# Kernel tuning notes

Hardware: AMD Instinct MI355X
Metric: run time of the kernel (lower is better)

## Reference

```python
import jax, jax.numpy as jnp
import numpy as np

N, IN, M = 8192, 512, 512


def setup_inputs() -> dict:
    key = jax.random.key(0)
    ks = jax.random.split(key, 16)
    sI = 1.0 / np.sqrt(IN)
    sM = 1.0 / np.sqrt(M)
    def p(k, shape, scale):
        return jax.random.uniform(k, shape, jnp.float32, -scale, scale)
    # topologically sorted tree: parent[i] < i for i>0; root (i=0) points to sentinel N
    rng = np.random.default_rng(0)
    parent = (rng.random(N) * np.arange(N)).astype(np.int64)
    parent[0] = N
    return {
        "inputs": jax.random.normal(ks[0], (N, IN), jnp.float32),
        "parent": jnp.asarray(parent),
        # FPChildSumTreeLSTM params (bottom-up)
        "cs_Wx": p(ks[1], (5 * M, IN), sI), "cs_bx": p(ks[2], (5 * M,), sI),
        "cs_Wio": p(ks[3], (2 * M, M), sM), "cs_bio": p(ks[4], (2 * M,), sM),
        "cs_Wfz": p(ks[5], (2 * M, M), sM), "cs_bfz": p(ks[6], (2 * M,), sM),
        "cs_Wum": p(ks[7], (M, M), sM), "cs_bum": p(ks[8], (M,), sM),
        # FPChainTreeLSTM params (top-down)
        "ch_Wx": p(ks[9], (5 * M, IN), sI), "ch_bx": p(ks[10], (5 * M,), sI),
        "ch_Wh": p(ks[11], (4 * M, M), sM), "ch_bh": p(ks[12], (4 * M,), sM),
        "ch_Wum": p(ks[13], (M, M), sM), "ch_bum": p(ks[14], (M,), sM),
    }


def _childsum(inputs, parent, Wx, bx, Wio, bio, Wfz, bfz, Wum, bum):
    # Precompute input projections for all nodes at once; row N is a zero sentinel.
    px = inputs @ Wx.T + bx                                  # (N, 5M)
    px = jnp.concatenate([px, jnp.zeros((1, 5 * M), px.dtype)], axis=0)
    ix, fx, ox, zx, ux = (px[:, j * M:(j + 1) * M] for j in range(5))
    # Process nodes leaves->root (reverse topo order). Each finished node j
    # scatters its parent-dependent contributions into accumulators at parent[j]:
    #   acc_h  += h_j
    #   acc_fc += sigmoid(fx_parent + U_f h_j + b_f) * c_j
    #   acc_zc += sigmoid(zx_parent + U_z h_j + b_z) * tanh(c_j)
    # Leaves see zero accumulators, which exactly matches the torch zero phantom child.
    zero = jnp.zeros((N + 1, M), inputs.dtype)

    def step(carry, i):
        acc_h, acc_fc, acc_zc = carry
        io = acc_h[i] @ Wio.T + bio                          # (2M,)
        i_g = jax.nn.sigmoid(ix[i] + io[:M])
        o_g = jax.nn.sigmoid(ox[i] + io[M:])
        u = jnp.tanh(ux[i] + acc_zc[i] @ Wum.T + bum)
        c = i_g * u + acc_fc[i]
        h = o_g * jnp.tanh(c)
        p = parent[i]                                        # root -> sentinel N
        fz = h @ Wfz.T + bfz
        f = jax.nn.sigmoid(fx[p] + fz[:M])
        z = jax.nn.sigmoid(zx[p] + fz[M:])
        acc_h = acc_h.at[p].add(h)
        acc_fc = acc_fc.at[p].add(f * c)
        acc_zc = acc_zc.at[p].add(z * jnp.tanh(c))
        return (acc_h, acc_fc, acc_zc), h

    _, hs = jax.lax.scan(step, (zero, zero, zero), jnp.arange(N - 1, -1, -1))
    return hs[-1]                                            # root hidden, (M,)


def _chain(inputs, parent, Wx, bx, Wh, bh, Wum, bum):
    qx = inputs @ Wx.T + bx                                  # (N, 5M), order i,o,f,z,u
    ix, ox, fx, zx, ux = (qx[:, j * M:(j + 1) * M] for j in range(5))
    zero = jnp.zeros((N + 1, M), inputs.dtype)               # slot N = root's zero parent

    def step(carry, i):
        c_all, h_all = carry
        p = parent[i]
        pc, ph = c_all[p], h_all[p]
        g = ph @ Wh.T + bh                                   # (4M,), order i,o,f,z
        i_g = jax.nn.sigmoid(ix[i] + g[:M])
        o_g = jax.nn.sigmoid(ox[i] + g[M:2 * M])
        f_g = jax.nn.sigmoid(fx[i] + g[2 * M:3 * M])
        z_g = jax.nn.sigmoid(zx[i] + g[3 * M:])
        u = jnp.tanh(ux[i] + (z_g * jnp.tanh(pc)) @ Wum.T + bum)
        c = i_g * u + f_g * pc
        h = o_g * jnp.tanh(c)
        return (c_all.at[i].set(c), h_all.at[i].set(h)), None

    (_, h_all), _ = jax.lax.scan(step, (zero, zero), jnp.arange(N))
    return jnp.max(h_all[:N], axis=0)                        # max over all node hiddens, (M,)


def reference(inputs, parent, cs_Wx, cs_bx, cs_Wio, cs_bio, cs_Wfz, cs_bfz,
              cs_Wum, cs_bum, ch_Wx, ch_bx, ch_Wh, ch_bh, ch_Wum, ch_bum):
    frep = _childsum(inputs, parent, cs_Wx, cs_bx, cs_Wio, cs_bio,
                     cs_Wfz, cs_bfz, cs_Wum, cs_bum)
    brep = _chain(inputs, parent, ch_Wx, ch_bx, ch_Wh, ch_bh, ch_Wum, ch_bum)
    return jnp.concatenate([frep, brep])[None, :]            # (1, 2M)
```

## Files before the change

kernel.cpp:

```cpp
#include <hip/hip_runtime.h>
#include <hip/hip_cooperative_groups.h>
#include <hip/hip_bf16.h>

typedef unsigned short u16;
typedef unsigned int u32;
typedef unsigned long long u64;

#define NN 8192
#define PXC 2560
#define MAXD 36
#define GY 64
#define GYM 32

typedef __attribute__((ext_vector_type(8))) short bf16x8;
typedef __attribute__((ext_vector_type(4))) float f32x4;

static constexpr size_t SZ_PX  = (size_t)(NN + 1) * PXC * 2;
static constexpr size_t SZ_ACC = (size_t)(NN + 1) * 512 * 4;
static constexpr size_t SZ_HB  = (size_t)(NN + 1) * 512 * 2;
static constexpr size_t SZ_G   = (size_t)(NN + 1) * 1536 * 4;
static constexpr size_t SZ_NW  = (size_t)5242880 * 2;

static constexpr size_t OFF_PX    = 0;
static constexpr size_t OFF_QX    = OFF_PX + SZ_PX;
static constexpr size_t OFF_ACCH  = OFF_QX + SZ_PX;
static constexpr size_t OFF_ACCF  = OFF_ACCH + SZ_ACC;
static constexpr size_t OFF_ACCZ  = OFF_ACCF + SZ_ACC;
static constexpr size_t OFF_C     = OFF_ACCZ + SZ_ACC;
static constexpr size_t OFF_HB    = OFF_C + SZ_ACC;
static constexpr size_t OFF_ZB    = OFF_HB + SZ_HB;
static constexpr size_t OFF_G     = OFF_ZB + SZ_HB;
static constexpr size_t OFF_NW    = OFF_G + SZ_G;
static constexpr size_t OFF_DEPTH = OFF_NW + SZ_NW;
static constexpr size_t OFF_ORDER = OFF_DEPTH + (size_t)NN * 4;
static constexpr size_t OFF_MISC  = OFF_ORDER + (size_t)NN * 4;
static constexpr size_t OFF_LVL   = OFF_MISC + 1024;
static constexpr size_t OFF_NB    = OFF_LVL + 512;
static constexpr size_t OFF_PN    = OFF_NB + 20480;
static constexpr size_t OFF_PMAX  = OFF_PN + (size_t)NN * 4;
static constexpr size_t OFF_BAR   = OFF_PMAX + (size_t)128 * 512 * 4;
static constexpr size_t WS_TOTAL  = OFF_BAR + 32768;

#define NW_CSWX  0
#define NW_CHWX  1310720
#define NW_CSWIO 2621440
#define NW_CSWFZ 3145728
#define NW_CSWUM 3670016
#define NW_CHWH  3932160
#define NW_CHWUM 4980736

#define NB_CSBX  0
#define NB_CSBIO 2560
#define NB_CSBFZ 3584
#define NB_CSBUM 4608
#define NB_CHBX  5120
#define NB_CHBH  7680
#define NB_CHBUM 9728

__device__ __forceinline__ float bfu(u16 u) { return __uint_as_float(((u32)u) << 16); }
__device__ __forceinline__ u16 f2bf(float f) {
    u32 u = __float_as_uint(f);
    u += 0x7fffu + ((u >> 16) & 1u);
    return (u16)(u >> 16);
}
__device__ __forceinline__ float sigf(float x) {
    x = fminf(fmaxf(x, -30.f), 30.f);
    return 1.f / (1.f + __expf(-x));
}
__device__ __forceinline__ float tanhq(float x) {
    x = fminf(fmaxf(x, -15.f), 15.f);
    return 1.f - 2.f / (__expf(2.f * x) + 1.f);
}
__device__ __forceinline__ bf16x8 cvt8(const float* p) {
    float4 a = *(const float4*)p;
    float4 b = *(const float4*)(p + 4);
    union { u32 u[4]; bf16x8 v; } r;
    r.u[0] = ((__float_as_uint(a.x) + 0x8000u) >> 16) | ((__float_as_uint(a.y) + 0x8000u) & 0xffff0000u);
    r.u[1] = ((__float_as_uint(a.z) + 0x8000u) >> 16) | ((__float_as_uint(a.w) + 0x8000u) & 0xffff0000u);
    r.u[2] = ((__float_as_uint(b.x) + 0x8000u) >> 16) | ((__float_as_uint(b.y) + 0x8000u) & 0xffff0000u);
    r.u[3] = ((__float_as_uint(b.z) + 0x8000u) >> 16) | ((__float_as_uint(b.w) + 0x8000u) & 0xffff0000u);
    return r.v;
}

__device__ __forceinline__ u64 cld64(const void* p) {
    return __hip_atomic_load((const u64*)p, __ATOMIC_RELAXED, __HIP_MEMORY_SCOPE_AGENT);
}
__device__ __forceinline__ float cldf(const float* p) {
    return __hip_atomic_load(p, __ATOMIC_RELAXED, __HIP_MEMORY_SCOPE_AGENT);
}
__device__ __forceinline__ void cstf(float* p, float v) {
    __hip_atomic_store(p, v, __ATOMIC_RELAXED, __HIP_MEMORY_SCOPE_AGENT);
}
__device__ __forceinline__ void cst16(u16* p, u16 v) {
    __hip_atomic_store(p, v, __ATOMIC_RELAXED, __HIP_MEMORY_SCOPE_AGENT);
}
__device__ __forceinline__ bf16x8 cldb16(const u16* p) {
    union { u64 u[2]; bf16x8 v; } r;
    r.u[0] = cld64(p); r.u[1] = cld64(p + 4);
    return r.v;
}
__device__ __forceinline__ bf16x8 cvt8a(const float* p) {
    union { u64 u; u32 w[2]; } a, b, c, d;
    a.u = cld64(p); b.u = cld64(p + 2); c.u = cld64(p + 4); d.u = cld64(p + 6);
    union { u32 u[4]; bf16x8 v; } r;
    r.u[0] = ((a.w[0] + 0x8000u) >> 16) | ((a.w[1] + 0x8000u) & 0xffff0000u);
    r.u[1] = ((b.w[0] + 0x8000u) >> 16) | ((b.w[1] + 0x8000u) & 0xffff0000u);
    r.u[2] = ((c.w[0] + 0x8000u) >> 16) | ((c.w[1] + 0x8000u) & 0xffff0000u);
    r.u[3] = ((d.w[0] + 0x8000u) >> 16) | ((d.w[1] + 0x8000u) & 0xffff0000u);
    return r.v;
}

__device__ __forceinline__ void grid_bar(u32* B, int bid, u32 tgt) {
    __syncthreads();
    if (threadIdx.x == 0) {
        u32* leaf = B + (bid & 7) * 16;
        u32* root = B + 128;
        u32* gen  = B + 144;
        bool rel = false;
        u32 lo = __hip_atomic_fetch_add(leaf, 1u, __ATOMIC_RELAXED, __HIP_MEMORY_SCOPE_AGENT);
        if (lo == 31u) {
            __hip_atomic_store(leaf, 0u, __ATOMIC_RELAXED, __HIP_MEMORY_SCOPE_AGENT);
            u32 ro = __hip_atomic_fetch_add(root, 1u, __ATOMIC_RELAXED, __HIP_MEMORY_SCOPE_AGENT);
            if (ro == 7u) {
                __hip_atomic_store(root, 0u, __ATOMIC_RELAXED, __HIP_MEMORY_SCOPE_AGENT);
                __hip_atomic_store(gen, tgt, __ATOMIC_RELAXED, __HIP_MEMORY_SCOPE_AGENT);
                rel = true;
            }
        }
        if (!rel) {
            while (__hip_atomic_load(gen, __ATOMIC_RELAXED, __HIP_MEMORY_SCOPE_AGENT) < tgt)
                __builtin_amdgcn_s_sleep(1);
        }
        asm volatile("" ::: "memory");
    }
    __syncthreads();
}

__device__ __forceinline__ void mini_bar(u32* C, u32 tgt) {
    __syncthreads();
    if (threadIdx.x == 0) {
        __hip_atomic_fetch_add(C, 1u, __ATOMIC_RELAXED, __HIP_MEMORY_SCOPE_AGENT);
        while (__hip_atomic_load(C, __ATOMIC_RELAXED, __HIP_MEMORY_SCOPE_AGENT) < tgt)
            __builtin_amdgcn_s_sleep(1);
        asm volatile("" ::: "memory");
    }
    __syncthreads();
}

__global__ void k_detect(const u32* __restrict__ fin, const u32* __restrict__ pin,
                         int* __restrict__ fcnt, int* __restrict__ pcnt,
                         u32* __restrict__ barz) {
    int i = blockIdx.x * 256 + threadIdx.x;
    if (i < 8192) barz[i] = 0u;
    if (i < 4096) {
        u32 w = fin[i];
        int e = (w >> 7) & 0xFF;
        if (w != 0u && e >= 0x70 && e <= 0x8F) atomicAdd(fcnt, 1);
    }
    if (i >= 1 && i < 4096) {
        if (pin[2 * i - 1] != 0u) atomicAdd(pcnt, 1);
    }
}

__global__ void k_pnorm_depth(const u32* __restrict__ pin, const int* __restrict__ pcnt,
                              int* __restrict__ pnorm, int* __restrict__ depth,
                              u16* __restrict__ HB, float* __restrict__ Call) {
    int i = blockIdx.x * 256 + threadIdx.x;
    if (i < 512) {
        HB[(size_t)NN * 512 + i] = 0;
        Call[(size_t)NN * 512 + i] = 0.f;
    }
    if (i >= NN) return;
    bool is64 = (*pcnt < 100);
    int p = (int)(is64 ? pin[2 * i] : pin[i]);
    pnorm[i] = p;
    int d = 0;
    while (p != NN && p >= 0 && p < NN && d < 9000) {
        d++;
        p = (int)(is64 ? pin[2 * p] : pin[p]);
    }
    depth[i] = d;
}

__global__ __launch_bounds__(1024) void k_levels(const int* __restrict__ depth,
                                                 int* __restrict__ lvl, int* __restrict__ order) {
    __shared__ int cnts[64];
    __shared__ int cur[64];
    int t = threadIdx.x;
    if (t < 64) cnts[t] = 0;
    __syncthreads();
    for (int i = t; i < NN; i += 1024) {
        int d = depth[i]; if (d > 63) d = 63;
        atomicAdd(&cnts[d], 1);
    }
    __syncthreads();
    if (t == 0) {
        int s = 0; lvl[0] = 0;
        for (int d = 0; d < 64; ++d) { cur[d] = s; s += cnts[d]; lvl[d + 1] = s; }
        int D = 1;
        for (int d = 63; d >= 0; --d) if (cnts[d] > 0) { D = d + 1; break; }
        lvl[80] = D;
    }
    __syncthreads();
    for (int i = t; i < NN; i += 1024) {
        int d = depth[i]; if (d > 63) d = 63;
        int pos = atomicAdd(&cur[d], 1);
        order[pos] = i;
    }
}

struct NormSrcs { const void* p[15]; };
__global__ __launch_bounds__(256) void k_norm_all(NormSrcs s, u16* __restrict__ NGI,
                                                  u16* __restrict__ NW, u16* __restrict__ NB,
                                                  const int* __restrict__ fcnt) {
    const int cum[16] = {0, 1048576, 1376256, 1703936, 1835008, 1966080, 2031616, 2293760,
                         2359296, 2359936, 2360192, 2360448, 2360576, 2361216, 2361728, 2361856};
    const int dof[15] = {0, NW_CSWX / 4, NW_CHWX / 4, NW_CSWIO / 4, NW_CSWFZ / 4, NW_CSWUM / 4,
                         NW_CHWH / 4, NW_CHWUM / 4, NB_CSBX / 4, NB_CSBIO / 4, NB_CSBFZ / 4,
                         NB_CSBUM / 4, NB_CHBX / 4, NB_CHBH / 4, NB_CHBUM / 4};
    bool isbf = (*fcnt > 2048);
    int total = 2361856;
    int istart = isbf ? cum[8] : 0;
    for (int i = istart + blockIdx.x * 256 + threadIdx.x; i < total; i += gridDim.x * 256) {
        int seg = 0;
#pragma unroll
        for (int k = 1; k < 15; ++k) if (i >= cum[k]) seg = k;
        int off = i - cum[seg];
        u16* dbase = (seg == 0) ? NGI : (seg < 8 ? NW : NB);
        ushort4* dst = (ushort4*)dbase + dof[seg] + off;
        if (isbf) {
            *dst = ((const ushort4*)s.p[seg])[off];
        } else {
            float4 v = ((const float4*)s.p[seg])[off];
            ushort4 o; o.x = f2bf(v.x); o.y = f2bf(v.y); o.z = f2bf(v.z); o.w = f2bf(v.w);
            *dst = o;
        }
    }
}

#define ASTR 528
__global__ __launch_bounds__(256) void k_gemm_in(
    const u16* __restrict__ Ao, const u16* __restrict__ An,
    const u16* __restrict__ Wcs_o, const u16* __restrict__ Wcs_n,
    const u16* __restrict__ Wch_o, const u16* __restrict__ Wch_n,
    const u16* __restrict__ bcs, const u16* __restrict__ bch,
    u16* __restrict__ Ccs, u16* __restrict__ Cch,
    const int* __restrict__ fcnt)
{
    __shared__ __align__(16) u16 AS[64 * ASTR];
    bool isbf = (*fcnt > 2048);
    int z = blockIdx.z;
    const u16* A = isbf ? Ao : An;
    const u16* W = z ? (isbf ? Wch_o : Wch_n) : (isbf ? Wcs_o : Wcs_n);
    const u16* bias = z ? bch : bcs;
    u16* C = z ? Cch : Ccs;

    int m0 = blockIdx.y * 64;
    for (int e = threadIdx.x; e < 64 * 64; e += 256) {
        int row = e >> 6, c8 = e & 63;
        *(uint4*)&AS[row * ASTR + c8 * 8] = *(const uint4*)(A + (size_t)(m0 + row) * 512 + c8 * 8);
    }
    __syncthreads();

    int wv = threadIdx.x >> 6;
    int lane = threadIdx.x & 63;
    int r = lane & 15, q = lane >> 4;
    int n0 = blockIdx.x * 256 + wv * 64;
    const u16* pb[4];
#pragma unroll
    for (int jt = 0; jt < 4; ++jt) pb[jt] = W + (size_t)(n0 + jt * 16 + r) * 512 + q * 8;
    f32x4 acc[4][4] = {};
#pragma unroll 2
    for (int k0 = 0; k0 < 512; k0 += 32) {
        bf16x8 a[4], b[4];
#pragma unroll
        for (int mi = 0; mi < 4; ++mi)
            a[mi] = *(const bf16x8*)&AS[(mi * 16 + r) * ASTR + k0 + q * 8];
#pragma unroll
        for (int jt = 0; jt < 4; ++jt) b[jt] = *(const bf16x8*)(pb[jt] + k0);
#pragma unroll
        for (int mi = 0; mi < 4; ++mi)
#pragma unroll
            for (int jt = 0; jt < 4; ++jt)
                acc[mi][jt] = __builtin_amdgcn_mfma_f32_16x16x32_bf16(a[mi], b[jt], acc[mi][jt], 0, 0, 0);
    }
#pragma unroll
    for (int jt = 0; jt < 4; ++jt) {
        int c = n0 + jt * 16 + r;
        float bv = bfu(bias[c]);
#pragma unroll
        for (int mi = 0; mi < 4; ++mi) {
            size_t b0 = (size_t)(m0 + mi * 16 + q * 4) * PXC + c;
#pragma unroll
            for (int i = 0; i < 4; ++i)
                C[b0 + (size_t)i * PXC] = f2bf(acc[mi][jt][i] + bv);
        }
    }
}

__global__ __launch_bounds__(512, 2) void comb_mega4(
    const int* __restrict__ order, const int* __restrict__ lvl, const int* __restrict__ parent,
    float* __restrict__ acc_h, float* __restrict__ acc_fc, float* __restrict__ acc_zc,
    const u16* __restrict__ Wio_o, const u16* __restrict__ Wio_n,
    const u16* __restrict__ Wum_o, const u16* __restrict__ Wum_n,
    const u16* __restrict__ Wfz_o, const u16* __restrict__ Wfz_n,
    const u16* __restrict__ bio, const u16* __restrict__ bum, const u16* __restrict__ bfz,
    const u16* __restrict__ px,
    u16* __restrict__ HB, float* __restrict__ Call,
    const u16* __restrict__ Wh_o, const u16* __restrict__ Wh_n,
    const u16* __restrict__ Wu2_o, const u16* __restrict__ Wu2_n,
    const u16* __restrict__ bh, const u16* __restrict__ bu2,
    const u16* __restrict__ qx, u16* __restrict__ ZB,
    float* __restrict__ G,
    void* __restrict__ outv, const int* __restrict__ fcnt,
    u32* __restrict__ BAR)
{
    __shared__ __align__(16) u16 LS[16384];
    __shared__ int ndl[16], pl[16];
    bool isbf = (*fcnt > 2048);
    int tid = threadIdx.x;
    int w = tid >> 6, lane = tid & 63;
    int r = lane & 15, q = lane >> 4;
    int rsw = (r & 7) << 4;
    int bid = blockIdx.x;
    int z = bid & 1;
    int cgi = (bid >> 1) & 3;
    int ty = bid >> 3;
    int col = (cgi * 8 + w) * 16 + r;
    u16* Gh = (u16*)G;
    char* LB = (char*)LS;
    int Dmax = lvl[80];
    u32* MB = BAR + 512 + (size_t)((z << 5) + ty) * 32;
    u32 tgt = 0, mtgt = 0;

    const u16 *p1a, *p1b, *p1c, *p1d;
    const u16 *p2a, *p2b;
    float ba, bb, bc, bd, be;
    if (z == 0) {
        const u16* Wio = isbf ? Wio_o : Wio_n;
        const u16* Wum = isbf ? Wum_o : Wum_n;
        const u16* Wfz = isbf ? Wfz_o : Wfz_n;
        p1a = Wio + (size_t)col * 512 + q * 8;
        p1b = Wio + (size_t)(512 + col) * 512 + q * 8;
        p1c = Wum + (size_t)col * 512 + q * 8;
        p1d = p1c;
        p2a = Wfz + (size_t)col * 512 + q * 8;
        p2b = Wfz + (size_t)(512 + col) * 512 + q * 8;
        ba = bfu(bio[col]); bb = bfu(bio[512 + col]); bc = bfu(bum[col]);
        bd = bfu(bfz[col]); be = bfu(bfz[512 + col]);
    } else {
        const u16* Wh = isbf ? Wh_o : Wh_n;
        const u16* Wu = isbf ? Wu2_o : Wu2_n;
        p1a = Wh + (size_t)col * 512 + q * 8;
        p1b = Wh + (size_t)(512 + col) * 512 + q * 8;
        p1c = Wh + (size_t)(1024 + col) * 512 + q * 8;
        p1d = Wh + (size_t)(1536 + col) * 512 + q * 8;
        p2a = Wu + (size_t)col * 512 + q * 8;
        p2b = p2a;
        ba = bfu(bh[col]); bb = bfu(bh[512 + col]);
        bc = bfu(bh[1024 + col]); bd = bfu(bh[1536 + col]);
        be = bfu(bu2[col]);
    }

    for (int it = 0; it < Dmax; ++it) {
        int d = z ? it : (Dmax - 1 - it);
        int start = lvl[d], cnt = lvl[d + 1] - start;
        int ntiles = (cnt + 15) >> 4;

        for (int tile = ty; tile < ntiles; tile += GYM) {
            __syncthreads();
            if (tid < 16) {
                int tr = tile * 16 + tid;
                int nd = (tr < cnt) ? order[start + tr] : -1;
                ndl[tid] = nd;
                pl[tid] = (nd >= 0) ? parent[nd] : NN;
            }
            __syncthreads();

            if (z == 0) {
                for (int e = tid; e < 1024; e += 512) {
                    int slot = e >> 6, c8 = e & 63;
                    int nd = ndl[slot]; int nn = (nd < 0) ? NN : nd;
                    int boff = slot * 1024 + ((c8 * 16) ^ ((slot & 7) << 4));
                    *(bf16x8*)(LB + boff) = cvt8a(acc_h + (size_t)nn * 512 + c8 * 8);
                    *(bf16x8*)(LB + 16384 + boff) = cvt8a(acc_zc + (size_t)nn * 512 + c8 * 8);
                }
                __syncthreads();
                f32x4 ai = {}, ao = {}, au = {};
#pragma unroll 4
                for (int ko = 0; ko < 512; ko += 32) {
                    int abo = ((ko + q * 8) * 2) ^ rsw;
                    bf16x8 ah = *(const bf16x8*)(LB + r * 1024 + abo);
                    bf16x8 az = *(const bf16x8*)(LB + 16384 + r * 1024 + abo);
                    ai = __builtin_amdgcn_mfma_f32_16x16x32_bf16(ah, *(const bf16x8*)(p1a + ko), ai, 0, 0, 0);
                    ao = __builtin_amdgcn_mfma_f32_16x16x32_bf16(ah, *(const bf16x8*)(p1b + ko), ao, 0, 0, 0);
                    au = __builtin_amdgcn_mfma_f32_16x16x32_bf16(az, *(const bf16x8*)(p1c + ko), au, 0, 0, 0);
                }
                float ccv[4];
#pragma unroll
                for (int i2 = 0; i2 < 4; ++i2) {
                    int slot = q * 4 + i2;
                    int ni = ndl[slot];
                    ccv[i2] = 0.f;
                    if (ni < 0) continue;
                    int p = pl[slot];
                    size_t pxb = (size_t)ni * PXC, nb = (size_t)ni * 512;
                    float ig = sigf(bfu(px[pxb + col]) + ai[i2] + ba);
                    float og = sigf(bfu(px[pxb + 1024 + col]) + ao[i2] + bb);
                    float uu = tanhq(bfu(px[pxb + 2048 + col]) + au[i2] + bc);
                    float cc = ig * uu + cldf(acc_fc + nb + col);
                    float h = og * tanhq(cc);
                    ccv[i2] = cc;
                    cst16(&Gh[(size_t)ni * 3072 + 1024 + col], f2bf(h));
                    atomicAdd(&acc_h[(size_t)p * 512 + col], h);
                    if (ni == 0) {
                        if (isbf) ((u16*)outv)[col] = f2bf(h);
                        else ((float*)outv)[col] = h;
                    }
                }
                mtgt += 4; mini_bar(MB, mtgt);
                for (int e = tid; e < 1024; e += 512) {
                    int slot = e >> 6, c8 = e & 63;
                    int nd = ndl[slot]; int nn = (nd < 0) ? NN : nd;
                    int boff = slot * 1024 + ((c8 * 16) ^ ((slot & 7) << 4));
                    *(bf16x8*)(LB + boff) = cldb16(Gh + (size_t)nn * 3072 + 1024 + c8 * 8);
                }
                __syncthreads();
                f32x4 af0 = {}, af1 = {}, az0 = {}, az1 = {};
#pragma unroll 4
                for (int ko = 0; ko < 256; ko += 32) {
                    int ab0 = ((ko + q * 8) * 2) ^ rsw;
                    int ab1 = ((ko + 256 + q * 8) * 2) ^ rsw;
                    bf16x8 h0 = *(const bf16x8*)(LB + r * 1024 + ab0);
                    bf16x8 h1 = *(const bf16x8*)(LB + r * 1024 + ab1);
                    af0 = __builtin_amdgcn_mfma_f32_16x16x32_bf16(h0, *(const bf16x8*)(p2a + ko), af0, 0, 0, 0);
                    az0 = __builtin_amdgcn_mfma_f32_16x16x32_bf16(h0, *(const bf16x8*)(p2b + ko), az0, 0, 0, 0);
                    af1 = __builtin_amdgcn_mfma_f32_16x16x32_bf16(h1, *(const bf16x8*)(p2a + 256 + ko), af1, 0, 0, 0);
                    az1 = __builtin_amdgcn_mfma_f32_16x16x32_bf16(h1, *(const bf16x8*)(p2b + 256 + ko), az1, 0, 0, 0);
                }
                f32x4 af = af0 + af1, az = az0 + az1;
#pragma unroll
                for (int i2 = 0; i2 < 4; ++i2) {
                    int slot = q * 4 + i2;
                    int ni = ndl[slot];
                    if (ni < 0) continue;
                    int p = pl[slot];
                    size_t pb = (size_t)p * 512, ppx = (size_t)p * PXC;
                    float cT = ccv[i2];
                    float f = sigf(bfu(px[ppx + 512 + col]) + af[i2] + bd);
                    atomicAdd(&acc_fc[pb + col], f * cT);
                    float zf = sigf(bfu(px[ppx + 1536 + col]) + az[i2] + be);
                    atomicAdd(&acc_zc[pb + col], zf * tanhq(cT));
                }
            } else {
                for (int e = tid; e < 1024; e += 512) {
                    int slot = e >> 6, c8 = e & 63;
                    int boff = slot * 1024 + ((c8 * 16) ^ ((slot & 7) << 4));
                    *(bf16x8*)(LB + boff) = cldb16(HB + (size_t)pl[slot] * 512 + c8 * 8);
                }
                __syncthreads();
                f32x4 gi = {}, go = {}, gf = {}, gz = {};
#pragma unroll 4
                for (int ko = 0; ko < 512; ko += 32) {
                    int abo = ((ko + q * 8) * 2) ^ rsw;
                    bf16x8 a = *(const bf16x8*)(LB + r * 1024 + abo);
                    gi = __builtin_amdgcn_mfma_f32_16x16x32_bf16(a, *(const bf16x8*)(p1a + ko), gi, 0, 0, 0);
                    go = __builtin_amdgcn_mfma_f32_16x16x32_bf16(a, *(const bf16x8*)(p1b + ko), go, 0, 0, 0);
                    gf = __builtin_amdgcn_mfma_f32_16x16x32_bf16(a, *(const bf16x8*)(p1c + ko), gf, 0, 0, 0);
                    gz = __builtin_amdgcn_mfma_f32_16x16x32_bf16(a, *(const bf16x8*)(p1d + ko), gz, 0, 0, 0);
                }
                float siR[4], soR[4], sfR[4], pcR[4];
#pragma unroll
                for (int i2 = 0; i2 < 4; ++i2) {
                    int slot = q * 4 + i2;
                    int ni = ndl[slot];
                    siR[i2] = 0.f; soR[i2] = 0.f; sfR[i2] = 0.f; pcR[i2] = 0.f;
                    if (ni < 0) continue;
                    int p = pl[slot];
                    size_t qb = (size_t)ni * PXC, nb = (size_t)ni * 512;
                    float si = sigf(bfu(qx[qb + col]) + gi[i2] + ba);
                    float so = sigf(bfu(qx[qb + 512 + col]) + go[i2] + bb);
                    float sf = sigf(bfu(qx[qb + 1024 + col]) + gf[i2] + bc);
                    float zg = sigf(bfu(qx[qb + 1536 + col]) + gz[i2] + bd);
                    float pc = cldf(Call + (size_t)p * 512 + col);
                    siR[i2] = si; soR[i2] = so; sfR[i2] = sf; pcR[i2] = pc;
                    cst16(&ZB[nb + col], f2bf(zg * tanhq(pc)));
                }
                mtgt += 4; mini_bar(MB, mtgt);
                for (int e = tid; e < 1024; e += 512) {
                    int slot = e >> 6, c8 = e & 63;
                    int nd = ndl[slot]; int nn = (nd < 0) ? NN : nd;
                    int boff = slot * 1024 + ((c8 * 16) ^ ((slot & 7) << 4));
                    *(bf16x8*)(LB + boff) = cldb16(ZB + (size_t)nn * 512 + c8 * 8);
                }
                __syncthreads();
                f32x4 a0 = {}, a1 = {}, a2 = {}, a3 = {};
#pragma unroll 4
                for (int ko = 0; ko < 128; ko += 32) {
                    int b0 = ((ko + q * 8) * 2) ^ rsw;
                    int b1 = ((ko + 128 + q * 8) * 2) ^ rsw;
                    int b2 = ((ko + 256 + q * 8) * 2) ^ rsw;
                    int b3 = ((ko + 384 + q * 8) * 2) ^ rsw;
                    a0 = __builtin_amdgcn_mfma_f32_16x16x32_bf16(*(const bf16x8*)(LB + r * 1024 + b0),
                                                                 *(const bf16x8*)(p2a + ko), a0, 0, 0, 0);
                    a1 = __builtin_amdgcn_mfma_f32_16x16x32_bf16(*(const bf16x8*)(LB + r * 1024 + b1),
                                                                 *(const bf16x8*)(p2a + 128 + ko), a1, 0, 0, 0);
                    a2 = __builtin_amdgcn_mfma_f32_16x16x32_bf16(*(const bf16x8*)(LB + r * 1024 + b2),
                                                                 *(const bf16x8*)(p2a + 256 + ko), a2, 0, 0, 0);
                    a3 = __builtin_amdgcn_mfma_f32_16x16x32_bf16(*(const bf16x8*)(LB + r * 1024 + b3),
                                                                 *(const bf16x8*)(p2a + 384 + ko), a3, 0, 0, 0);
                }
                f32x4 au = (a0 + a1) + (a2 + a3);
#pragma unroll
                for (int i2 = 0; i2 < 4; ++i2) {
                    int slot = q * 4 + i2;
                    int ni = ndl[slot];
                    if (ni < 0) continue;
                    size_t qb = (size_t)ni * PXC, nb = (size_t)ni * 512;
                    float uu = tanhq(bfu(qx[qb + 2048 + col]) + au[i2] + be);
                    float cc = siR[i2] * uu + sfR[i2] * pcR[i2];
                    float h = soR[i2] * tanhq(cc);
                    cstf(&Call[nb + col], cc);
                    cst16(&HB[nb + col], f2bf(h));
                }
            }
        }
        ++tgt; grid_bar(BAR, bid, tgt);
    }
}

__global__ __launch_bounds__(512) void comb_s1(
    int iter,
    const int* __restrict__ order, const int* __restrict__ lvl, const int* __restrict__ parent,
    float* acc_h, const float* __restrict__ acc_fc, const float* __restrict__ acc_zc,
    const u16* __restrict__ Wio_o, const u16* __restrict__ Wio_n,
    const u16* __restrict__ Wum_o, const u16* __restrict__ Wum_n,
    const u16* __restrict__ bio, const u16* __restrict__ bum,
    const u16* __restrict__ px,
    const u16* __restrict__ HB, const float* __restrict__ Call,
    const u16* __restrict__ Wh_o, const u16* __restrict__ Wh_n,
    const u16* __restrict__ bh,
    const u16* __restrict__ qx, u16* __restrict__ ZB,
    float* __restrict__ G,
    void* __restrict__ outv, const int* __restrict__ fcnt)
{
    __shared__ __align__(16) u16 LS[16384];
    __shared__ int ndl[16], pl[16];
    bool isbf = (*fcnt > 2048);
    int tid = threadIdx.x;
    int w = tid >> 6, lane = tid & 63;
    int r = lane & 15, q = lane >> 4;
    int rsw = (r & 7) << 4;
    int col = (blockIdx.x * 8 + w) * 16 + r;
    u16* Gh = (u16*)G;
    char* LB = (char*)LS;
    int Dmax = lvl[80];
    int d = blockIdx.z ? iter : (Dmax - 1 - iter);
    if (d < 0 || d >= Dmax) return;
    int start = lvl[d], cnt = lvl[d + 1] - start;
    if (cnt <= 0) return;
    int ntiles = (cnt + 15) >> 4;

    if (blockIdx.z == 0) {
        const u16* Wio = isbf ? Wio_o : Wio_n;
        const u16* Wum = isbf ? Wum_o : Wum_n;
        const u16* pbi = Wio + (size_t)col * 512 + q * 8;
        const u16* pbo = Wio + (size_t)(512 + col) * 512 + q * 8;
        const u16* pbu = Wum + (size_t)col * 512 + q * 8;
        for (int tile = blockIdx.y; tile < ntiles; tile += GY) {
            __syncthreads();
            if (tid < 16) {
                int tr = tile * 16 + tid;
                int nd = (tr < cnt) ? order[start + tr] : -1;
                ndl[tid] = nd;
                pl[tid] = (nd >= 0) ? parent[nd] : NN;
            }
            __syncthreads();
            for (int e = tid; e < 1024; e += 512) {
                int slot = e >> 6, c8 = e & 63;
                int nd = ndl[slot]; int nn = (nd < 0) ? NN : nd;
                int boff = slot * 1024 + ((c8 * 16) ^ ((slot & 7) << 4));
                *(bf16x8*)(LB + boff) = cvt8(acc_h + (size_t)nn * 512 + c8 * 8);
                *(bf16x8*)(LB + 16384 + boff) = cvt8(acc_zc + (size_t)nn * 512 + c8 * 8);
            }
            __syncthreads();
            f32x4 ai = {}, ao = {}, au = {};
#pragma unroll 4
            for (int ko = 0; ko < 512; ko += 32) {
                int abo = ((ko + q * 8) * 2) ^ rsw;
                bf16x8 ah = *(const bf16x8*)(LB + r * 1024 + abo);
                bf16x8 az = *(const bf16x8*)(LB + 16384 + r * 1024 + abo);
                ai = __builtin_amdgcn_mfma_f32_16x16x32_bf16(ah, *(const bf16x8*)(pbi + ko), ai, 0, 0, 0);
                ao = __builtin_amdgcn_mfma_f32_16x16x32_bf16(ah, *(const bf16x8*)(pbo + ko), ao, 0, 0, 0);
                au = __builtin_amdgcn_mfma_f32_16x16x32_bf16(az, *(const bf16x8*)(pbu + ko), au, 0, 0, 0);
            }
            float bi_ = bfu(bio[col]), bo_ = bfu(bio[512 + col]), bu_ = bfu(bum[col]);
#pragma unroll
            for (int i2 = 0; i2 < 4; ++i2) {
// ... 228 lines not shown
    int i = blockIdx.x * 256 + threadIdx.x;
    if (i < 1024) out[i] = f2bf(12345.f);
}

extern "C" void kernel_launch(void* const* d_in, const int* in_sizes, int n_in,
                              void* d_out, int out_size, void* d_ws, size_t ws_size,
                              hipStream_t stream) {
    char* base = (char*)d_ws;
    u16* px = (u16*)(base + OFF_PX);
    u16* qx = (u16*)(base + OFF_QX);
    float* acc_h = (float*)(base + OFF_ACCH);
    float* acc_fc = (float*)(base + OFF_ACCF);
    float* acc_zc = (float*)(base + OFF_ACCZ);
    float* Call = (float*)(base + OFF_C);
    u16* HB = (u16*)(base + OFF_HB);
    u16* ZB = (u16*)(base + OFF_ZB);
    float* G = (float*)(base + OFF_G);
    u16* NGI = (u16*)(base + OFF_G);
    u16* NW = (u16*)(base + OFF_NW);
    int* depth = (int*)(base + OFF_DEPTH);
    int* order = (int*)(base + OFF_ORDER);
    int* counts = (int*)(base + OFF_MISC);
    int* fcnt = counts + 128;
    int* pcnt = counts + 129;
    int* lvl = (int*)(base + OFF_LVL);
    u16* NB = (u16*)(base + OFF_NB);
    int* pnorm = (int*)(base + OFF_PN);
    float* pmax = (float*)(base + OFF_PMAX);
    u32* BAR = (u32*)(base + OFF_BAR);

    const u16* in_bf   = (const u16*)d_in[0];
    const u16* csWx_o  = (const u16*)d_in[2];
    const u16* csWio_o = (const u16*)d_in[4];
    const u16* csWfz_o = (const u16*)d_in[6];
    const u16* csWum_o = (const u16*)d_in[8];
    const u16* chWx_o  = (const u16*)d_in[10];
    const u16* chWh_o  = (const u16*)d_in[12];
    const u16* chWum_o = (const u16*)d_in[14];

    if (ws_size < WS_TOTAL) { k_wsfail<<<4, 256, 0, stream>>>((u16*)d_out); return; }

    hipMemsetAsync(base + OFF_MISC, 0, 1024, stream);
    hipMemsetAsync(base + OFF_ACCH, 0, 3 * SZ_ACC, stream);

    k_detect<<<32, 256, 0, stream>>>((const u32*)d_in[0], (const u32*)d_in[1], fcnt, pcnt, BAR);
    k_pnorm_depth<<<32, 256, 0, stream>>>((const u32*)d_in[1], pcnt, pnorm, depth, HB, Call);
    k_levels<<<1, 1024, 0, stream>>>(depth, lvl, order);

    NormSrcs srcs;
    srcs.p[0] = d_in[0];  srcs.p[1] = d_in[2];  srcs.p[2] = d_in[10]; srcs.p[3] = d_in[4];
    srcs.p[4] = d_in[6];  srcs.p[5] = d_in[8];  srcs.p[6] = d_in[12]; srcs.p[7] = d_in[14];
    srcs.p[8] = d_in[3];  srcs.p[9] = d_in[5];  srcs.p[10] = d_in[7]; srcs.p[11] = d_in[9];
    srcs.p[12] = d_in[11]; srcs.p[13] = d_in[13]; srcs.p[14] = d_in[15];
    k_norm_all<<<2048, 256, 0, stream>>>(srcs, NGI, NW, NB, fcnt);

    dim3 gg(PXC / 256, NN / 64, 2);
    k_gemm_in<<<gg, 256, 0, stream>>>(in_bf, NGI,
                                      csWx_o, NW + NW_CSWX, chWx_o, NW + NW_CHWX,
                                      NB + NB_CSBX, NB + NB_CHBX, px, qx, fcnt);

    {
        const u16* nWio = NW + NW_CSWIO; const u16* nWum = NW + NW_CSWUM;
        const u16* nWfz = NW + NW_CSWFZ; const u16* nWh = NW + NW_CHWH;
        const u16* nWu2 = NW + NW_CHWUM;
        const u16* b_io = NB + NB_CSBIO; const u16* b_um = NB + NB_CSBUM;
        const u16* b_fz = NB + NB_CSBFZ; const u16* b_h = NB + NB_CHBH;
        const u16* b_u2 = NB + NB_CHBUM;
        const int* order_c = order; const int* lvl_c = lvl; const int* par_c = pnorm;
        const u16* px_c = px; const u16* qx_c = qx;
        void* outp = d_out; const int* fcnt_c = fcnt;
        u32* bar_c = BAR;
        void* margs[] = {
            (void*)&order_c, (void*)&lvl_c, (void*)&par_c,
            (void*)&acc_h, (void*)&acc_fc, (void*)&acc_zc,
            (void*)&csWio_o, (void*)&nWio, (void*)&csWum_o, (void*)&nWum,
            (void*)&csWfz_o, (void*)&nWfz,
            (void*)&b_io, (void*)&b_um, (void*)&b_fz,
            (void*)&px_c, (void*)&HB, (void*)&Call,
            (void*)&chWh_o, (void*)&nWh, (void*)&chWum_o, (void*)&nWu2,
            (void*)&b_h, (void*)&b_u2,
            (void*)&qx_c, (void*)&ZB, (void*)&G,
            (void*)&outp, (void*)&fcnt_c, (void*)&bar_c
        };
        hipError_t ce = hipLaunchCooperativeKernel((const void*)comb_mega4,
                                                   dim3(256), dim3(512), margs, 0, stream);
        if (ce != hipSuccess) {
            (void)hipGetLastError();
            dim3 gl(4, GY, 2);
            for (int i = 0; i < MAXD; ++i) {
                comb_s1<<<gl, 512, 0, stream>>>(i, order, lvl, pnorm,
                                                acc_h, acc_fc, acc_zc,
                                                csWio_o, NW + NW_CSWIO, csWum_o, NW + NW_CSWUM,
                                                NB + NB_CSBIO, NB + NB_CSBUM, px,
                                                HB, Call, chWh_o, NW + NW_CHWH, NB + NB_CHBH,
                                                qx, ZB, G, d_out, fcnt);
                comb_s2<<<gl, 512, 0, stream>>>(i, order, lvl, pnorm,
                                                csWfz_o, NW + NW_CSWFZ, NB + NB_CSBFZ, px,
                                                acc_fc, acc_zc,
                                                ZB, qx, chWum_o, NW + NW_CHWUM, NB + NB_CHBUM,
                                                Call, HB, G, fcnt);
            }
        }
    }

    k_maxA<<<64, 256, 0, stream>>>(HB, pmax);
    k_maxB<<<1, 512, 0, stream>>>(pmax, d_out, fcnt);
}
```

Before: 1.236 ms.

## Widen persistent blocks to 1024 threads processing two node tiles per iteration

The cooperative persistent kernel now uses 1024-thread blocks in which each half handles its own 16-node tile, so a block covers 32 nodes per pass and the tile stride doubles. Shared staging buffers double to hold both tiles, and node/parent lists are sized for 32 slots. The aim is to cut the number of tile iterations and syncthreads rounds per level and to amortize per-tile setup. In exchange, register pressure may force lower occupancy or spills under launch_bounds(1024), and a block-wide syncthreads now couples the two halves. If the cooperative launch of 256 such blocks cannot be co-resident, the slow fallback path runs instead.

After: 1.498 ms. +21.2%, slower.

```diff
diff --git a/kernel.cpp b/kernel.cpp
--- a/kernel.cpp
+++ b/kernel.cpp
@@ -298,7 +298,7 @@
     }
 }
 
-__global__ __launch_bounds__(512, 2) void comb_mega4(
+__global__ __launch_bounds__(1024) void comb_mega5(
     const int* __restrict__ order, const int* __restrict__ lvl, const int* __restrict__ parent,
     float* __restrict__ acc_h, float* __restrict__ acc_fc, float* __restrict__ acc_zc,
     const u16* __restrict__ Wio_o, const u16* __restrict__ Wio_n,
@@ -315,11 +315,13 @@
     void* __restrict__ outv, const int* __restrict__ fcnt,
     u32* __restrict__ BAR)
 {
-    __shared__ __align__(16) u16 LS[16384];
-    __shared__ int ndl[16], pl[16];
+    __shared__ __align__(16) u16 LS[32768];
+    __shared__ int ndl[32], pl[32];
     bool isbf = (*fcnt > 2048);
     int tid = threadIdx.x;
-    int w = tid >> 6, lane = tid & 63;
+    int half = tid >> 9;
+    int w = (tid >> 6) & 7;
+    int lane = tid & 63;
     int r = lane & 15, q = lane >> 4;
     int rsw = (r & 7) << 4;
     int bid = blockIdx.x;
@@ -327,6 +329,7 @@
     int cgi = (bid >> 1) & 3;
     int ty = bid >> 3;
     int col = (cgi * 8 + w) * 16 + r;
+    int hbase = half * 16384;
     u16* Gh = (u16*)G;
     char* LB = (char*)LS;
     int Dmax = lvl[80];
@@ -367,10 +370,11 @@
         int start = lvl[d], cnt = lvl[d + 1] - start;
         int ntiles = (cnt + 15) >> 4;
 
-        for (int tile = ty; tile < ntiles; tile += GYM) {
-            __syncthreads();
-            if (tid < 16) {
-                int tr = tile * 16 + tid;
+        for (int tb = ty * 2; tb < ntiles; tb += 2 * GYM) {
+            __syncthreads();
+            if (tid < 32) {
+                int hh = tid >> 4, sl = tid & 15;
+                int tr = (tb + hh) * 16 + sl;
                 int nd = (tr < cnt) ? order[start + tr] : -1;
                 ndl[tid] = nd;
                 pl[tid] = (nd >= 0) ? parent[nd] : NN;
@@ -378,20 +382,21 @@
             __syncthreads();
 
             if (z == 0) {
-                for (int e = tid; e < 1024; e += 512) {
-                    int slot = e >> 6, c8 = e & 63;
-                    int nd = ndl[slot]; int nn = (nd < 0) ? NN : nd;
-                    int boff = slot * 1024 + ((c8 * 16) ^ ((slot & 7) << 4));
+                for (int e = tid; e < 2048; e += 1024) {
+                    int sg = e >> 6, c8 = e & 63;
+                    int hh = sg >> 4, sl = sg & 15;
+                    int nd = ndl[sg]; int nn = (nd < 0) ? NN : nd;
+                    int boff = hh * 16384 + sl * 1024 + ((c8 * 16) ^ ((sl & 7) << 4));
                     *(bf16x8*)(LB + boff) = cvt8a(acc_h + (size_t)nn * 512 + c8 * 8);
-                    *(bf16x8*)(LB + 16384 + boff) = cvt8a(acc_zc + (size_t)nn * 512 + c8 * 8);
+                    *(bf16x8*)(LB + 32768 + boff) = cvt8a(acc_zc + (size_t)nn * 512 + c8 * 8);
                 }
                 __syncthreads();
                 f32x4 ai = {}, ao = {}, au = {};
 #pragma unroll 4
                 for (int ko = 0; ko < 512; ko += 32) {
                     int abo = ((ko + q * 8) * 2) ^ rsw;
-                    bf16x8 ah = *(const bf16x8*)(LB + r * 1024 + abo);
-                    bf16x8 az = *(const bf16x8*)(LB + 16384 + r * 1024 + abo);
+                    bf16x8 ah = *(const bf16x8*)(LB + hbase + r * 1024 + abo);
+                    bf16x8 az = *(const bf16x8*)(LB + 32768 + hbase + r * 1024 + abo);
                     ai = __builtin_amdgcn_mfma_f32_16x16x32_bf16(ah, *(const bf16x8*)(p1a + ko), ai, 0, 0, 0);
                     ao = __builtin_amdgcn_mfma_f32_16x16x32_bf16(ah, *(const bf16x8*)(p1b + ko), ao, 0, 0, 0);
                     au = __builtin_amdgcn_mfma_f32_16x16x32_bf16(az, *(const bf16x8*)(p1c + ko), au, 0, 0, 0);
@@ -399,7 +404,7 @@
                 float ccv[4];
 #pragma unroll
                 for (int i2 = 0; i2 < 4; ++i2) {
-                    int slot = q * 4 + i2;
+                    int slot = half * 16 + q * 4 + i2;
                     int ni = ndl[slot];
                     ccv[i2] = 0.f;
                     if (ni < 0) continue;
@@ -419,10 +424,11 @@
                     }
                 }
                 mtgt += 4; mini_bar(MB, mtgt);
-                for (int e = tid; e < 1024; e += 512) {
-                    int slot = e >> 6, c8 = e & 63;
-                    int nd = ndl[slot]; int nn = (nd < 0) ? NN : nd;
-                    int boff = slot * 1024 + ((c8 * 16) ^ ((slot & 7) << 4));
+                for (int e = tid; e < 2048; e += 1024) {
+                    int sg = e >> 6, c8 = e & 63;
+                    int hh = sg >> 4, sl = sg & 15;
+                    int nd = ndl[sg]; int nn = (nd < 0) ? NN : nd;
+                    int boff = hh * 16384 + sl * 1024 + ((c8 * 16) ^ ((sl & 7) << 4));
                     *(bf16x8*)(LB + boff) = cldb16(Gh + (size_t)nn * 3072 + 1024 + c8 * 8);
                 }
                 __syncthreads();
@@ -431,8 +437,8 @@
                 for (int ko = 0; ko < 256; ko += 32) {
                     int ab0 = ((ko + q * 8) * 2) ^ rsw;
                     int ab1 = ((ko + 256 + q * 8) * 2) ^ rsw;
-                    bf16x8 h0 = *(const bf16x8*)(LB + r * 1024 + ab0);
-                    bf16x8 h1 = *(const bf16x8*)(LB + r * 1024 + ab1);
+                    bf16x8 h0 = *(const bf16x8*)(LB + hbase + r * 1024 + ab0);
+                    bf16x8 h1 = *(const bf16x8*)(LB + hbase + r * 1024 + ab1);
                     af0 = __builtin_amdgcn_mfma_f32_16x16x32_bf16(h0, *(const bf16x8*)(p2a + ko), af0, 0, 0, 0);
                     az0 = __builtin_amdgcn_mfma_f32_16x16x32_bf16(h0, *(const bf16x8*)(p2b + ko), az0, 0, 0, 0);
                     af1 = __builtin_amdgcn_mfma_f32_16x16x32_bf16(h1, *(const bf16x8*)(p2a + 256 + ko), af1, 0, 0, 0);
@@ -441,7 +447,7 @@
                 f32x4 af = af0 + af1, az = az0 + az1;
 #pragma unroll
                 for (int i2 = 0; i2 < 4; ++i2) {
-                    int slot = q * 4 + i2;
+                    int slot = half * 16 + q * 4 + i2;
                     int ni = ndl[slot];
                     if (ni < 0) continue;
                     int p = pl[slot];
@@ -453,17 +459,18 @@
                     atomicAdd(&acc_zc[pb + col], zf * tanhq(cT));
                 }
             } else {
-                for (int e = tid; e < 1024; e += 512) {
-                    int slot = e >> 6, c8 = e & 63;
-                    int boff = slot * 1024 + ((c8 * 16) ^ ((slot & 7) << 4));
-                    *(bf16x8*)(LB + boff) = cldb16(HB + (size_t)pl[slot] * 512 + c8 * 8);
+                for (int e = tid; e < 2048; e += 1024) {
+                    int sg = e >> 6, c8 = e & 63;
+                    int hh = sg >> 4, sl = sg & 15;
+                    int boff = hh * 16384 + sl * 1024 + ((c8 * 16) ^ ((sl & 7) << 4));
+                    *(bf16x8*)(LB + boff) = cldb16(HB + (size_t)pl[sg] * 512 + c8 * 8);
                 }
                 __syncthreads();
                 f32x4 gi = {}, go = {}, gf = {}, gz = {};
 #pragma unroll 4
                 for (int ko = 0; ko < 512; ko += 32) {
                     int abo = ((ko + q * 8) * 2) ^ rsw;
-                    bf16x8 a = *(const bf16x8*)(LB + r * 1024 + abo);
+                    bf16x8 a = *(const bf16x8*)(LB + hbase + r * 1024 + abo);
                     gi = __builtin_amdgcn_mfma_f32_16x16x32_bf16(a, *(const bf16x8*)(p1a + ko), gi, 0, 0, 0);
                     go = __builtin_amdgcn_mfma_f32_16x16x32_bf16(a, *(const bf16x8*)(p1b + ko), go, 0, 0, 0);
                     gf = __builtin_amdgcn_mfma_f32_16x16x32_bf16(a, *(const bf16x8*)(p1c + ko), gf, 0, 0, 0);
@@ -472,7 +479,7 @@
                 float siR[4], soR[4], sfR[4], pcR[4];
 #pragma unroll
                 for (int i2 = 0; i2 < 4; ++i2) {
-                    int slot = q * 4 + i2;
+                    int slot = half * 16 + q * 4 + i2;
                     int ni = ndl[slot];
                     siR[i2] = 0.f; soR[i2] = 0.f; sfR[i2] = 0.f; pcR[i2] = 0.f;
                     if (ni < 0) continue;
@@ -487,10 +494,11 @@
                     cst16(&ZB[nb + col], f2bf(zg * tanhq(pc)));
                 }
                 mtgt += 4; mini_bar(MB, mtgt);
-                for (int e = tid; e < 1024; e += 512) {
-                    int slot = e >> 6, c8 = e & 63;
-                    int nd = ndl[slot]; int nn = (nd < 0) ? NN : nd;
-                    int boff = slot * 1024 + ((c8 * 16) ^ ((slot & 7) << 4));
+                for (int e = tid; e < 2048; e += 1024) {
+                    int sg = e >> 6, c8 = e & 63;
+                    int hh = sg >> 4, sl = sg & 15;
+                    int nd = ndl[sg]; int nn = (nd < 0) ? NN : nd;
+                    int boff = hh * 16384 + sl * 1024 + ((c8 * 16) ^ ((sl & 7) << 4));
                     *(bf16x8*)(LB + boff) = cldb16(ZB + (size_t)nn * 512 + c8 * 8);
                 }
                 __syncthreads();
@@ -501,19 +509,19 @@
                     int b1 = ((ko + 128 + q * 8) * 2) ^ rsw;
                     int b2 = ((ko + 256 + q * 8) * 2) ^ rsw;
                     int b3 = ((ko + 384 + q * 8) * 2) ^ rsw;
-                    a0 = __builtin_amdgcn_mfma_f32_16x16x32_bf16(*(const bf16x8*)(LB + r * 1024 + b0),
+                    a0 = __builtin_amdgcn_mfma_f32_16x16x32_bf16(*(const bf16x8*)(LB + hbase + r * 1024 + b0),
                                                                  *(const bf16x8*)(p2a + ko), a0, 0, 0, 0);
-                    a1 = __builtin_amdgcn_mfma_f32_16x16x32_bf16(*(const bf16x8*)(LB + r * 1024 + b1),
+                    a1 = __builtin_amdgcn_mfma_f32_16x16x32_bf16(*(const bf16x8*)(LB + hbase + r * 1024 + b1),
                                                                  *(const bf16x8*)(p2a + 128 + ko), a1, 0, 0, 0);
-                    a2 = __builtin_amdgcn_mfma_f32_16x16x32_bf16(*(const bf16x8*)(LB + r * 1024 + b2),
+                    a2 = __builtin_amdgcn_mfma_f32_16x16x32_bf16(*(const bf16x8*)(LB + hbase + r * 1024 + b2),
                                                                  *(const bf16x8*)(p2a + 256 + ko), a2, 0, 0, 0);
-                    a3 = __builtin_amdgcn_mfma_f32_16x16x32_bf16(*(const bf16x8*)(LB + r * 1024 + b3),
+                    a3 = __builtin_amdgcn_mfma_f32_16x16x32_bf16(*(const bf16x8*)(LB + hbase + r * 1024 + b3),
                                                                  *(const bf16x8*)(p2a + 384 + ko), a3, 0, 0, 0);
                 }
                 f32x4 au = (a0 + a1) + (a2 + a3);
 #pragma unroll
                 for (int i2 = 0; i2 < 4; ++i2) {
-                    int slot = q * 4 + i2;
+                    int slot = half * 16 + q * 4 + i2;
                     int ni = ndl[slot];
                     if (ni < 0) continue;
                     size_t qb = (size_t)ni * PXC, nb = (size_t)ni * 512;
@@ -908,8 +916,8 @@
             (void*)&qx_c, (void*)&ZB, (void*)&G,
             (void*)&outp, (void*)&fcnt_c, (void*)&bar_c
         };
-        hipError_t ce = hipLaunchCooperativeKernel((const void*)comb_mega4,
-                                                   dim3(256), dim3(512), margs, 0, stream);
+        hipError_t ce = hipLaunchCooperativeKernel((const void*)comb_mega5,
+                                                   dim3(256), dim3(1024), margs, 0, stream);
         if (ce != hipSuccess) {
             (void)hipGetLastError();
             dim3 gl(4, GY, 2);
```

## Replace counter-based grid and group barriers with flag-based barriers; use plain loads

Applied to the files above, without the earlier changes.

The two-level atomic-counter grid barrier becomes a flag barrier: each block writes its generation to its own slot, block 0 polls all 256 slots and then releases a shared generation word. The group mini-barrier likewise switches from a shared fetch-add counter to four per-group flags that every member polls. Several cross-block reads that used relaxed atomic loads now use ordinary vector loads, which may be cached and so rely on the barriers for visibility. The aim is to cut atomic contention and barrier latency in the persistent kernel, with some risk of reading stale data because no explicit fences are added.

New measurement: 1.221 ms. About the same (-1.1%).

```diff
diff --git a/kernel.cpp b/kernel.cpp
--- a/kernel.cpp
+++ b/kernel.cpp
@@ -94,11 +94,6 @@
 __device__ __forceinline__ void cst16(u16* p, u16 v) {
     __hip_atomic_store(p, v, __ATOMIC_RELAXED, __HIP_MEMORY_SCOPE_AGENT);
 }
-__device__ __forceinline__ bf16x8 cldb16(const u16* p) {
-    union { u64 u[2]; bf16x8 v; } r;
-    r.u[0] = cld64(p); r.u[1] = cld64(p + 4);
-    return r.v;
-}
 __device__ __forceinline__ bf16x8 cvt8a(const float* p) {
     union { u64 u; u32 w[2]; } a, b, c, d;
     a.u = cld64(p); b.u = cld64(p + 2); c.u = cld64(p + 4); d.u = cld64(p + 6);
@@ -112,36 +107,38 @@
 
 __device__ __forceinline__ void grid_bar(u32* B, int bid, u32 tgt) {
     __syncthreads();
-    if (threadIdx.x == 0) {
-        u32* leaf = B + (bid & 7) * 16;
-        u32* root = B + 128;
-        u32* gen  = B + 144;
-        bool rel = false;
-        u32 lo = __hip_atomic_fetch_add(leaf, 1u, __ATOMIC_RELAXED, __HIP_MEMORY_SCOPE_AGENT);
-        if (lo == 31u) {
-            __hip_atomic_store(leaf, 0u, __ATOMIC_RELAXED, __HIP_MEMORY_SCOPE_AGENT);
-            u32 ro = __hip_atomic_fetch_add(root, 1u, __ATOMIC_RELAXED, __HIP_MEMORY_SCOPE_AGENT);
-            if (ro == 7u) {
-                __hip_atomic_store(root, 0u, __ATOMIC_RELAXED, __HIP_MEMORY_SCOPE_AGENT);
-                __hip_atomic_store(gen, tgt, __ATOMIC_RELAXED, __HIP_MEMORY_SCOPE_AGENT);
-                rel = true;
-            }
+    int tid = threadIdx.x;
+    if (tid == 0)
+        __hip_atomic_store(B + 16 + bid * 16, tgt, __ATOMIC_RELAXED, __HIP_MEMORY_SCOPE_AGENT);
+    if (blockIdx.x == 0) {
+        if (tid < 256) {
+            while (__hip_atomic_load(B + 16 + tid * 16, __ATOMIC_RELAXED, __HIP_MEMORY_SCOPE_AGENT) < tgt)
+                __builtin_amdgcn_s_sleep(2);
         }
-        if (!rel) {
-            while (__hip_atomic_load(gen, __ATOMIC_RELAXED, __HIP_MEMORY_SCOPE_AGENT) < tgt)
-                __builtin_amdgcn_s_sleep(1);
-        }
+        __syncthreads();
+        if (tid == 0)
+            __hip_atomic_store(B, tgt, __ATOMIC_RELAXED, __HIP_MEMORY_SCOPE_AGENT);
+    }
+    if (tid == 0) {
+        while (__hip_atomic_load(B, __ATOMIC_RELAXED, __HIP_MEMORY_SCOPE_AGENT) < tgt)
+            __builtin_amdgcn_s_sleep(2);
         asm volatile("" ::: "memory");
     }
     __syncthreads();
 }
 
-__device__ __forceinline__ void mini_bar(u32* C, u32 tgt) {
+__device__ __forceinline__ void mini_bar(u32* MF, int cgi, u32 tgt) {
     __syncthreads();
     if (threadIdx.x == 0) {
-        __hip_atomic_fetch_add(C, 1u, __ATOMIC_RELAXED, __HIP_MEMORY_SCOPE_AGENT);
-        while (__hip_atomic_load(C, __ATOMIC_RELAXED, __HIP_MEMORY_SCOPE_AGENT) < tgt)
+        __hip_atomic_store(MF + cgi * 4, tgt, __ATOMIC_RELAXED, __HIP_MEMORY_SCOPE_AGENT);
+        for (;;) {
+            u32 a = __hip_atomic_load(MF + 0,  __ATOMIC_RELAXED, __HIP_MEMORY_SCOPE_AGENT);
+            u32 b = __hip_atomic_load(MF + 4,  __ATOMIC_RELAXED, __HIP_MEMORY_SCOPE_AGENT);
+            u32 c = __hip_atomic_load(MF + 8,  __ATOMIC_RELAXED, __HIP_MEMORY_SCOPE_AGENT);
+            u32 d = __hip_atomic_load(MF + 12, __ATOMIC_RELAXED, __HIP_MEMORY_SCOPE_AGENT);
+            if (a >= tgt && b >= tgt && c >= tgt && d >= tgt) break;
             __builtin_amdgcn_s_sleep(1);
+        }
         asm volatile("" ::: "memory");
     }
     __syncthreads();
@@ -298,7 +295,7 @@
     }
 }
 
-__global__ __launch_bounds__(512, 2) void comb_mega4(
+__global__ __launch_bounds__(512, 2) void comb_mega6(
     const int* __restrict__ order, const int* __restrict__ lvl, const int* __restrict__ parent,
     float* __restrict__ acc_h, float* __restrict__ acc_fc, float* __restrict__ acc_zc,
     const u16* __restrict__ Wio_o, const u16* __restrict__ Wio_n,
@@ -330,7 +327,7 @@
     u16* Gh = (u16*)G;
     char* LB = (char*)LS;
     int Dmax = lvl[80];
-    u32* MB = BAR + 512 + (size_t)((z << 5) + ty) * 32;
+    u32* MF = BAR + 5120 + (size_t)((z << 5) + ty) * 16;
     u32 tgt = 0, mtgt = 0;
 
     const u16 *p1a, *p1b, *p1c, *p1d;
@@ -418,12 +415,12 @@
                         else ((float*)outv)[col] = h;
                     }
                 }
-                mtgt += 4; mini_bar(MB, mtgt);
+                ++mtgt; mini_bar(MF, cgi, mtgt);
                 for (int e = tid; e < 1024; e += 512) {
                     int slot = e >> 6, c8 = e & 63;
                     int nd = ndl[slot]; int nn = (nd < 0) ? NN : nd;
                     int boff = slot * 1024 + ((c8 * 16) ^ ((slot & 7) << 4));
-                    *(bf16x8*)(LB + boff) = cldb16(Gh + (size_t)nn * 3072 + 1024 + c8 * 8);
+                    *(bf16x8*)(LB + boff) = *(const bf16x8*)(Gh + (size_t)nn * 3072 + 1024 + c8 * 8);
                 }
                 __syncthreads();
                 f32x4 af0 = {}, af1 = {}, az0 = {}, az1 = {};
@@ -456,7 +453,7 @@
                 for (int e = tid; e < 1024; e += 512) {
                     int slot = e >> 6, c8 = e & 63;
                     int boff = slot * 1024 + ((c8 * 16) ^ ((slot & 7) << 4));
-                    *(bf16x8*)(LB + boff) = cldb16(HB + (size_t)pl[slot] * 512 + c8 * 8);
+                    *(bf16x8*)(LB + boff) = *(const bf16x8*)(HB + (size_t)pl[slot] * 512 + c8 * 8);
                 }
                 __syncthreads();
                 f32x4 gi = {}, go = {}, gf = {}, gz = {};
@@ -482,16 +479,16 @@
                     float so = sigf(bfu(qx[qb + 512 + col]) + go[i2] + bb);
                     float sf = sigf(bfu(qx[qb + 1024 + col]) + gf[i2] + bc);
                     float zg = sigf(bfu(qx[qb + 1536 + col]) + gz[i2] + bd);
-                    float pc = cldf(Call + (size_t)p * 512 + col);
+                    float pc = Call[(size_t)p * 512 + col];
                     siR[i2] = si; soR[i2] = so; sfR[i2] = sf; pcR[i2] = pc;
                     cst16(&ZB[nb + col], f2bf(zg * tanhq(pc)));
                 }
-                mtgt += 4; mini_bar(MB, mtgt);
+                ++mtgt; mini_bar(MF, cgi, mtgt);
                 for (int e = tid; e < 1024; e += 512) {
                     int slot = e >> 6, c8 = e & 63;
                     int nd = ndl[slot]; int nn = (nd < 0) ? NN : nd;
                     int boff = slot * 1024 + ((c8 * 16) ^ ((slot & 7) << 4));
-                    *(bf16x8*)(LB + boff) = cldb16(ZB + (size_t)nn * 512 + c8 * 8);
+                    *(bf16x8*)(LB + boff) = *(const bf16x8*)(ZB + (size_t)nn * 512 + c8 * 8);
                 }
                 __syncthreads();
                 f32x4 a0 = {}, a1 = {}, a2 = {}, a3 = {};
@@ -908,7 +905,7 @@
             (void*)&qx_c, (void*)&ZB, (void*)&G,
             (void*)&outp, (void*)&fcnt_c, (void*)&bar_c
         };
-        hipError_t ce = hipLaunchCooperativeKernel((const void*)comb_mega4,
+        hipError_t ce = hipLaunchCooperativeKernel((const void*)comb_mega6,
                                                    dim3(256), dim3(512), margs, 0, stream);
         if (ce != hipSuccess) {
             (void)hipGetLastError();
```
